# Performance work log

Hardware: AMD Instinct MI355X
Metric: run time of the kernel (lower is better)

The kernel has to match this reference:

```python
import math
import jax, jax.numpy as jnp
import numpy as np

B, T, S = 2, 2048, 2048
D_MODEL, N_HEADS = 1024, 16
HEAD_DIM = D_MODEL // N_HEADS
OUT_DIM = 1024


def setup_inputs() -> dict:
    key = jax.random.key(0)
    ks = jax.random.split(key, 6)
    q = jax.random.normal(ks[0], (B, T, D_MODEL), dtype=jnp.float32)
    k = jax.random.normal(ks[1], (B, S, D_MODEL), dtype=jnp.float32)
    v = jax.random.normal(ks[2], (B, S, D_MODEL), dtype=jnp.float32)
    rel_pos_bias = jax.random.normal(ks[3], (T, S, N_HEADS), dtype=jnp.float32)
    # shared qkv projection weight (torch ModuleList([Linear]*3) aliases one module)
    lim = 1.0 / math.sqrt(D_MODEL)
    Wqkv = jax.random.uniform(ks[4], (D_MODEL, D_MODEL), minval=-lim, maxval=lim, dtype=jnp.float32)
    Wout = jax.random.uniform(ks[5], (OUT_DIM, D_MODEL), minval=-lim, maxval=lim, dtype=jnp.float32)
    logit_scale = jnp.full((N_HEADS, 1, 1), math.log(10.0), dtype=jnp.float32)
    return {"q": q, "k": k, "v": v, "rel_pos_bias": rel_pos_bias,
            "Wqkv": Wqkv, "Wout": Wout, "logit_scale": logit_scale}


def _l2norm(x, eps=1e-12):
    # matches torch F.normalize(dim=-1)
    n = jnp.sqrt(jnp.sum(x * x, axis=-1, keepdims=True))
    return x / jnp.maximum(n, eps)


def reference(q, k, v, rel_pos_bias, Wqkv, Wout, logit_scale):
    # shared qkv projection (Linear, no bias): x @ W.T
    qp = q @ Wqkv.T
    kp = k @ Wqkv.T
    vp = v @ Wqkv.T
    # [B, H, T, Dh]
    qh = qp.reshape(B, T, N_HEADS, HEAD_DIM).transpose(0, 2, 1, 3)
    kh = kp.reshape(B, S, N_HEADS, HEAD_DIM).transpose(0, 2, 1, 3)
    vh = vp.reshape(B, S, N_HEADS, HEAD_DIM).transpose(0, 2, 1, 3)
    # cosine attention with clamped learned logit scale
    scale = jnp.exp(jnp.minimum(logit_scale, math.log(100.0)))  # [H,1,1]
    attn = jnp.einsum('bhtd,bhsd->bhts', _l2norm(qh), _l2norm(kh)) * scale
    # rel_pos_bias [T,S,H] -> [H,T,S], broadcast over batch
    attn = attn + rel_pos_bias.transpose(2, 0, 1)
    attn = jax.nn.softmax(attn, axis=-1)
    vals = jnp.einsum('bhts,bhsd->bhtd', attn, vh)
    vals = vals.transpose(0, 2, 1, 3).reshape(B, T, D_MODEL)
    return vals @ Wout.T
```

## Files before the change

### kernel.cpp

```cpp
#include <hip/hip_runtime.h>
#include <stdint.h>

typedef unsigned short u16;
using bf16x8 = __attribute__((ext_vector_type(8))) __bf16;
using f32x4  = __attribute__((ext_vector_type(4))) float;
using u16x8  = __attribute__((ext_vector_type(8))) u16;
using u16x4  = __attribute__((ext_vector_type(4))) u16;
using i32x4  = __attribute__((ext_vector_type(4))) int;

#define BB 2
#define TT 2048
#define SQ 2048
#define DM 1024
#define NH 16
#define HD 64
#define LOG2E 1.44269504088896340736f

__device__ __forceinline__ float bf2f(u16 u) {
  uint32_t x = ((uint32_t)u) << 16;
  return __builtin_bit_cast(float, x);
}
__device__ __forceinline__ u16 f2bf(float f) {
  uint32_t x = __builtin_bit_cast(uint32_t, f);
  x += 0x7fffu + ((x >> 16) & 1u);
  return (u16)(x >> 16);
}
__device__ __forceinline__ int cvt_pk_bf16(float lo, float hi) {
  int r;
  asm("v_cvt_pk_bf16_f32 %0, %1, %2" : "=v"(r) : "v"(lo), "v"(hi));
  return r;
}

typedef __attribute__((address_space(1))) void gvoid;
typedef __attribute__((address_space(3))) void lvoid;
__device__ __forceinline__ void g2l16(const void* g, void* l) {
  __builtin_amdgcn_global_load_lds((gvoid*)g, (lvoid*)l, 16, 0, 0);
}

__global__ __launch_bounds__(256) void convert_all(
    const float* __restrict__ q, const float* __restrict__ k,
    const float* __restrict__ v, const float* __restrict__ wq,
    const float* __restrict__ wo, u16* __restrict__ qc, u16* __restrict__ kc,
    u16* __restrict__ vc, u16* __restrict__ wqc, u16* __restrict__ woc) {
  const float* src;
  u16* dst;
  int n8;
  switch (blockIdx.y) {
    case 0:  src = q;  dst = qc;  n8 = 4096 * 1024 / 8; break;
    case 1:  src = k;  dst = kc;  n8 = 4096 * 1024 / 8; break;
    case 2:  src = v;  dst = vc;  n8 = 4096 * 1024 / 8; break;
    case 3:  src = wq; dst = wqc; n8 = 1024 * 1024 / 8; break;
    default: src = wo; dst = woc; n8 = 1024 * 1024 / 8; break;
  }
  int i = blockIdx.x * 256 + threadIdx.x;
  if (i >= n8) return;
  f32x4 a = ((const f32x4*)src)[(size_t)i * 2];
  f32x4 b = ((const f32x4*)src)[(size_t)i * 2 + 1];
  u16x8 o;
#pragma unroll
  for (int j = 0; j < 4; ++j) { o[j] = f2bf(a[j]); o[4 + j] = f2bf(b[j]); }
  ((u16x8*)dst)[i] = o;
}

template <typename OutT>
__device__ __forceinline__ void gemm_body(const u16* __restrict__ A,
                                          const u16* __restrict__ W,
                                          OutT* __restrict__ C,
                                          const float* __restrict__ ls,
                                          int norm_mode) {
  const int n0 = blockIdx.x * 128;
  const int m0 = blockIdx.y * 128;
  const int tid = threadIdx.x;
  const int w = tid >> 6, lane = tid & 63;
  const int l15 = lane & 15, lg = lane >> 4;
  const int wr = w >> 1, wc = w & 1;

  __shared__ u16 ldsA[16 * 512];
  __shared__ u16 ldsB[16 * 512];

  f32x4 acc[4][4];
#pragma unroll
  for (int i = 0; i < 4; ++i)
#pragma unroll
    for (int j = 0; j < 4; ++j) acc[i][j] = (f32x4){0.f, 0.f, 0.f, 0.f};

  for (int kt = 0; kt < 1024; kt += 64) {
#pragma unroll
    for (int u = 0; u < 4; ++u) {
      int f = w * 4 + u;
      int mt = f >> 1, ks = f & 1;
      g2l16(A + (size_t)(m0 + mt * 16 + l15) * 1024 + kt + ks * 32 + lg * 8,
            &ldsA[f * 512]);
      g2l16(W + (size_t)(n0 + mt * 16 + l15) * 1024 + kt + ks * 32 + lg * 8,
            &ldsB[f * 512]);
    }
    __syncthreads();
#pragma unroll
    for (int ks = 0; ks < 2; ++ks) {
      bf16x8 a[4], b[4];
#pragma unroll
      for (int i = 0; i < 4; ++i)
        a[i] = *(const bf16x8*)&ldsA[((wr * 4 + i) * 2 + ks) * 512 + lane * 8];
#pragma unroll
      for (int j = 0; j < 4; ++j)
        b[j] = *(const bf16x8*)&ldsB[((wc * 4 + j) * 2 + ks) * 512 + lane * 8];
#pragma unroll
      for (int i = 0; i < 4; ++i)
#pragma unroll
        for (int j = 0; j < 4; ++j)
          acc[i][j] = __builtin_amdgcn_mfma_f32_16x16x32_bf16(a[i], b[j],
                                                              acc[i][j], 0, 0, 0);
    }
    __syncthreads();
  }

  if (norm_mode < 2) {
    float sc = 1.0f;
    if (norm_mode == 0)
      sc = __expf(fminf(ls[(n0 >> 6) + wc], 4.60517019f)) * LOG2E;
#pragma unroll
    for (int i = 0; i < 4; ++i)
#pragma unroll
      for (int r = 0; r < 4; ++r) {
        float ss = 0.f;
#pragma unroll
        for (int j = 0; j < 4; ++j) ss += acc[i][j][r] * acc[i][j][r];
#pragma unroll
        for (int d = 1; d < 16; d <<= 1) ss += __shfl_xor(ss, d, 64);
        float f = sc / fmaxf(sqrtf(ss), 1e-12f);
#pragma unroll
        for (int j = 0; j < 4; ++j) acc[i][j][r] *= f;
      }
  }

#pragma unroll
  for (int i = 0; i < 4; ++i) {
    int row0 = m0 + (wr * 4 + i) * 16 + lg * 4;
#pragma unroll
    for (int j = 0; j < 4; ++j) {
      int col = n0 + (wc * 4 + j) * 16 + l15;
#pragma unroll
      for (int r = 0; r < 4; ++r) {
        if constexpr (sizeof(OutT) == 2)
          C[(size_t)(row0 + r) * 1024 + col] = f2bf(acc[i][j][r]);
        else
          C[(size_t)(row0 + r) * 1024 + col] = acc[i][j][r];
      }
    }
  }
}

__global__ __launch_bounds__(256, 2) void gemm_qkv(
    const u16* __restrict__ q, const u16* __restrict__ k,
    const u16* __restrict__ v, const u16* __restrict__ W,
    const float* __restrict__ ls,
    u16* __restrict__ qp, u16* __restrict__ kp, u16* __restrict__ vp) {
  const u16* A;
  u16* C;
  if (blockIdx.z == 0) { A = q; C = qp; }
  else if (blockIdx.z == 1) { A = k; C = kp; }
  else { A = v; C = vp; }
  gemm_body<u16>(A, W, C, ls, blockIdx.z);
}

__global__ __launch_bounds__(256, 2) void gemm_out(const u16* __restrict__ A,
                                                   const u16* __restrict__ W,
                                                   float* __restrict__ C) {
  gemm_body<float>(A, W, C, nullptr, 2);
}

__global__ __launch_bounds__(256) void transpose_v(const u16* __restrict__ vp,
                                                   u16* __restrict__ vt) {
  int st = blockIdx.x;
  int bh = blockIdx.y;
  __shared__ u16 lds[64][72];
  int tid = threadIdx.x;
  int s = tid >> 2, c0 = (tid & 3) * 16;
  int b = bh >> 4, h = bh & 15;
  const u16* src = vp + (size_t)(b * SQ + st * 64 + s) * 1024 + h * 64 + c0;
  u16x8 r0 = *(const u16x8*)src;
  u16x8 r1 = *(const u16x8*)(src + 8);
#pragma unroll
  for (int j = 0; j < 8; ++j) { lds[s][c0 + j] = r0[j]; lds[s][c0 + 8 + j] = r1[j]; }
  __syncthreads();
  int d = tid >> 2, sc = (tid & 3) * 16;
  u16x8 o0, o1;
#pragma unroll
  for (int j = 0; j < 8; ++j) { o0[j] = lds[sc + j][d]; o1[j] = lds[sc + 8 + j][d]; }
  u16* dst = vt + (size_t)(bh * 64 + d) * SQ + st * 64 + sc;
  *(u16x8*)dst = o0;
  *((u16x8*)(dst + 8)) = o1;
}

__global__ __launch_bounds__(256) void transpose_bias(const float* __restrict__ bias,
                                                      u16* __restrict__ bt) {
  int t = blockIdx.y;
  int s0 = blockIdx.x * 512;
  __shared__ u16 lds[16][520];
  int tid = threadIdx.x;
  const float* src = bias + ((size_t)t * SQ + s0 + tid * 2) * 16;
  float v[32];
#pragma unroll
  for (int j = 0; j < 8; ++j) {
    f32x4 r = ((const f32x4*)src)[j];
#pragma unroll
    for (int e = 0; e < 4; ++e) v[j * 4 + e] = r[e];
  }
  int sl = tid * 2;
#pragma unroll
  for (int e = 0; e < 32; ++e) lds[e & 15][sl + (e >> 4)] = f2bf(v[e] * LOG2E);
  __syncthreads();
  int h = tid >> 4, sc = (tid & 15) * 32;
  u16* dst = bt + ((size_t)h * TT + t) * SQ + s0 + sc;
#pragma unroll
  for (int j = 0; j < 4; ++j) {
    u16x8 o;
#pragma unroll
    for (int e = 0; e < 8; ++e) o[e] = lds[h][sc + j * 8 + e];
    *((u16x8*)(dst + j * 8)) = o;
  }
}

__global__ __launch_bounds__(256, 2) void flash_attn(
    const u16* __restrict__ qn, const u16* __restrict__ kn,
    const u16* __restrict__ vt, const u16* __restrict__ bt,
    u16* __restrict__ av) {
  const int h = blockIdx.x >> 1, b = blockIdx.x & 1, qt = blockIdx.y;
  const int tid = threadIdx.x, w = tid >> 6, lane = tid & 63;
  const int l15 = lane & 15, lg = lane >> 4;

  __shared__ u16 ldsK[2][16 * 512];
  __shared__ u16 ldsV[2][16 * 512];

  const int t0 = qt * 64 + w * 16;

  bf16x8 qf[2];
  {
    const u16* qb = qn + (size_t)(b * TT + t0 + l15) * 1024 + h * 64 + lg * 8;
    qf[0] = *(const bf16x8*)qb;
    qf[1] = *(const bf16x8*)(qb + 32);
  }

  f32x4 o[4];
#pragma unroll
  for (int n = 0; n < 4; ++n) o[n] = (f32x4){0.f, 0.f, 0.f, 0.f};
  float li = 0.f;

  const u16* kb = kn + (size_t)(b * SQ) * 1024 + h * 64;
  const u16* vb = vt + (size_t)((b * NH + h) * 64) * SQ;
  const u16* bbl = bt + ((size_t)h * TT + t0 + l15) * SQ + lg * 4;

#define STAGE(bufi, stg)                                                       \
  {                                                                            \
    _Pragma("unroll") for (int u_ = 0; u_ < 4; ++u_) {                         \
      int f_ = w * 4 + u_;                                                     \
      int nt_ = f_ >> 1, ks_ = f_ & 1;                                         \
      g2l16(kb + (size_t)((stg) + nt_ * 16 + l15) * 1024 + ks_ * 32 + lg * 8,  \
            &ldsK[bufi][f_ * 512]);                                            \
      int j_ = f_ >> 2, k2_ = f_ & 3;                                          \
      g2l16(vb + (size_t)(j_ * 16 + l15) * SQ + (stg) + k2_ * 32 + lg * 8,     \
            &ldsV[bufi][f_ * 512]);                                            \
    }                                                                          \
  }

  STAGE(0, 0);

  for (int it = 0; it < 16; ++it) {
    const int cur = it & 1;
    const int st = it * 128;

    u16x4 bv[8];
#pragma unroll
    for (int nt = 0; nt < 8; ++nt)
      bv[nt] = *(const u16x4*)(bbl + st + nt * 16);
    asm volatile("" ::: "memory");

    if (it < 15) {
      STAGE(cur ^ 1, st + 128);
      asm volatile("s_waitcnt vmcnt(16)" ::: "memory");
    } else {
      asm volatile("s_waitcnt vmcnt(8)" ::: "memory");
    }
    __builtin_amdgcn_s_barrier();

    f32x4 sacc[8];
#pragma unroll
    for (int nt = 0; nt < 8; ++nt) {
      sacc[nt] = (f32x4){0.f, 0.f, 0.f, 0.f};
#pragma unroll
      for (int ks = 0; ks < 2; ++ks)
        sacc[nt] = __builtin_amdgcn_mfma_f32_16x16x32_bf16(
            *(const bf16x8*)&ldsK[cur][(nt * 2 + ks) * 512 + lane * 8],
            qf[ks], sacc[nt], 0, 0, 0);
    }

    int pk[8][2];
#pragma unroll
    for (int nt = 0; nt < 8; ++nt) {
      float p0 = __builtin_amdgcn_exp2f(sacc[nt][0] + bf2f(bv[nt][0]));
      float p1 = __builtin_amdgcn_exp2f(sacc[nt][1] + bf2f(bv[nt][1]));
      float p2 = __builtin_amdgcn_exp2f(sacc[nt][2] + bf2f(bv[nt][2]));
      float p3 = __builtin_amdgcn_exp2f(sacc[nt][3] + bf2f(bv[nt][3]));
      li += (p0 + p1) + (p2 + p3);
      pk[nt][0] = cvt_pk_bf16(p0, p1);
      pk[nt][1] = cvt_pk_bf16(p2, p3);
    }

#pragma unroll
    for (int ks2 = 0; ks2 < 4; ++ks2) {
      auto a0 = __builtin_amdgcn_permlane32_swap(pk[2 * ks2][0],
                                                 pk[2 * ks2 + 1][0], false, false);
      auto w0 = __builtin_amdgcn_permlane16_swap(a0[0], a0[1], false, false);
      auto a1 = __builtin_amdgcn_permlane32_swap(pk[2 * ks2][1],
                                                 pk[2 * ks2 + 1][1], false, false);
      auto w1 = __builtin_amdgcn_permlane16_swap(a1[0], a1[1], false, false);
      i32x4 pw = (i32x4){(int)w0[0], (int)w1[0], (int)w0[1], (int)w1[1]};
      bf16x8 pf = __builtin_bit_cast(bf16x8, pw);
#pragma unroll
      for (int j = 0; j < 4; ++j)
        o[j] = __builtin_amdgcn_mfma_f32_16x16x32_bf16(
            pf, *(const bf16x8*)&ldsV[cur][(j * 4 + ks2) * 512 + lane * 8],
            o[j], 0, 0, 0);
    }
    if (it < 15) __builtin_amdgcn_s_barrier();
  }
#undef STAGE

  li += __shfl_xor(li, 16, 64);
  li += __shfl_xor(li, 32, 64);
  float inv[4];
#pragma unroll
  for (int r = 0; r < 4; ++r) inv[r] = 1.0f / __shfl(li, lg * 4 + r, 64);

#pragma unroll
  for (int j = 0; j < 4; ++j)
#pragma unroll
    for (int r = 0; r < 4; ++r) {
      size_t row = (size_t)(b * TT + t0 + lg * 4 + r);
      av[row * 1024 + h * 64 + j * 16 + l15] = f2bf(o[j][r] * inv[r]);
    }
}

extern "C" void kernel_launch(void* const* d_in, const int* in_sizes, int n_in,
                              void* d_out, int out_size, void* d_ws, size_t ws_size,
                              hipStream_t stream) {
  const float* q    = (const float*)d_in[0];
  const float* k    = (const float*)d_in[1];
  const float* v    = (const float*)d_in[2];
  const float* bias = (const float*)d_in[3];
  const float* Wqkv = (const float*)d_in[4];
  const float* Wout = (const float*)d_in[5];
  const float* ls   = (const float*)d_in[6];
  float* out = (float*)d_out;

  char* ws = (char*)d_ws;
  u16* qc = (u16*)(ws);
  u16* kc = (u16*)(ws + (size_t)(8  << 20));
  u16* vc = (u16*)(ws + (size_t)(16 << 20));
  u16* Wq = (u16*)(ws + (size_t)(24 << 20));
  u16* Wo = (u16*)(ws + (size_t)(26 << 20));
  u16* qn = (u16*)(ws + (size_t)(28 << 20));
  u16* kn = (u16*)(ws + (size_t)(36 << 20));
  u16* av = (u16*)(ws + (size_t)(44 << 20));
  u16* vtb = (u16*)(ws + (size_t)(52 << 20));
  u16* bt  = (u16*)(ws + (size_t)(60 << 20));

  dim3 blk(256);
  transpose_bias<<<dim3(4, 2048), blk, 0, stream>>>(bias, bt);
  convert_all<<<dim3(2048, 5), blk, 0, stream>>>(q, k, v, Wqkv, Wout,
                                                 qc, kc, vc, Wq, Wo);

  gemm_qkv<<<dim3(8, 32, 3), blk, 0, stream>>>(qc, kc, vc, Wq, ls, qn, kn, av);
  transpose_v<<<dim3(32, 32), blk, 0, stream>>>(av, vtb);
  flash_attn<<<dim3(32, 32), blk, 0, stream>>>(qn, kn, vtb, bt, av);
  gemm_out<<<dim3(8, 32), blk, 0, stream>>>(av, Wo, out);
}
```

Before: 650.1 us.

## Merge both batches into one 512-thread attention block; coalesce bias transpose loads

The flash attention kernel now processes both batch elements for one head and query tile in a single 512-thread block, with separate K/V LDS buffers per batch. The likely aim is to share each bias tile read between the two batches within one block and to halve the block count. The bias transpose kernel also changes its read pattern so adjacent threads load consecutive 16-byte chunks, giving coalesced global reads. LDS use per block doubles, which may limit occupancy, and the barriers now synchronise eight waves instead of four.

After: 672.7 us. +3.5%, slower.

```diff
diff --git a/kernel.cpp b/kernel.cpp
--- a/kernel.cpp
+++ b/kernel.cpp
@@ -198,17 +198,16 @@
   int s0 = blockIdx.x * 512;
   __shared__ u16 lds[16][520];
   int tid = threadIdx.x;
-  const float* src = bias + ((size_t)t * SQ + s0 + tid * 2) * 16;
-  float v[32];
-#pragma unroll
-  for (int j = 0; j < 8; ++j) {
-    f32x4 r = ((const f32x4*)src)[j];
-#pragma unroll
-    for (int e = 0; e < 4; ++e) v[j * 4 + e] = r[e];
-  }
-  int sl = tid * 2;
-#pragma unroll
-  for (int e = 0; e < 32; ++e) lds[e & 15][sl + (e >> 4)] = f2bf(v[e] * LOG2E);
+  const float* src = bias + ((size_t)t * SQ + s0) * 16;
+  int h0 = (tid & 3) * 4;
+  int sr = tid >> 2;
+#pragma unroll
+  for (int p = 0; p < 8; ++p) {
+    f32x4 r = *(const f32x4*)(src + p * 1024 + tid * 4);
+#pragma unroll
+    for (int e = 0; e < 4; ++e)
+      lds[h0 + e][p * 64 + sr] = f2bf(r[e] * LOG2E);
+  }
   __syncthreads();
   int h = tid >> 4, sc = (tid & 15) * 32;
   u16* dst = bt + ((size_t)h * TT + t) * SQ + s0 + sc;
@@ -221,16 +220,18 @@
   }
 }
 
-__global__ __launch_bounds__(256, 2) void flash_attn(
+__global__ __launch_bounds__(512, 2) void flash_attn(
     const u16* __restrict__ qn, const u16* __restrict__ kn,
     const u16* __restrict__ vt, const u16* __restrict__ bt,
     u16* __restrict__ av) {
-  const int h = blockIdx.x >> 1, b = blockIdx.x & 1, qt = blockIdx.y;
-  const int tid = threadIdx.x, w = tid >> 6, lane = tid & 63;
+  const int h = blockIdx.x, qt = blockIdx.y;
+  const int tid = threadIdx.x, lane = tid & 63;
+  const int wAll = tid >> 6;
+  const int b = wAll >> 2, w = wAll & 3;
   const int l15 = lane & 15, lg = lane >> 4;
 
-  __shared__ u16 ldsK[2][16 * 512];
-  __shared__ u16 ldsV[2][16 * 512];
+  __shared__ u16 ldsK[2][2][16 * 512];
+  __shared__ u16 ldsV[2][2][16 * 512];
 
   const int t0 = qt * 64 + w * 16;
 
@@ -256,10 +257,10 @@
       int f_ = w * 4 + u_;                                                     \
       int nt_ = f_ >> 1, ks_ = f_ & 1;                                         \
       g2l16(kb + (size_t)((stg) + nt_ * 16 + l15) * 1024 + ks_ * 32 + lg * 8,  \
-            &ldsK[bufi][f_ * 512]);                                            \
+            &ldsK[bufi][b][f_ * 512]);                                         \
       int j_ = f_ >> 2, k2_ = f_ & 3;                                          \
       g2l16(vb + (size_t)(j_ * 16 + l15) * SQ + (stg) + k2_ * 32 + lg * 8,     \
-            &ldsV[bufi][f_ * 512]);                                            \
+            &ldsV[bufi][b][f_ * 512]);                                         \
     }                                                                          \
   }
 
@@ -290,7 +291,7 @@
 #pragma unroll
       for (int ks = 0; ks < 2; ++ks)
         sacc[nt] = __builtin_amdgcn_mfma_f32_16x16x32_bf16(
-            *(const bf16x8*)&ldsK[cur][(nt * 2 + ks) * 512 + lane * 8],
+            *(const bf16x8*)&ldsK[cur][b][(nt * 2 + ks) * 512 + lane * 8],
             qf[ks], sacc[nt], 0, 0, 0);
     }
 
@@ -319,7 +320,7 @@
 #pragma unroll
       for (int j = 0; j < 4; ++j)
         o[j] = __builtin_amdgcn_mfma_f32_16x16x32_bf16(
-            pf, *(const bf16x8*)&ldsV[cur][(j * 4 + ks2) * 512 + lane * 8],
+            pf, *(const bf16x8*)&ldsV[cur][b][(j * 4 + ks2) * 512 + lane * 8],
             o[j], 0, 0, 0);
     }
     if (it < 15) __builtin_amdgcn_s_barrier();
@@ -372,6 +373,6 @@
 
   gemm_qkv<<<dim3(8, 32, 3), blk, 0, stream>>>(qc, kc, vc, Wq, ls, qn, kn, av);
   transpose_v<<<dim3(32, 32), blk, 0, stream>>>(av, vtb);
-  flash_attn<<<dim3(32, 32), blk, 0, stream>>>(qn, kn, vtb, bt, av);
+  flash_attn<<<dim3(16, 32), dim3(512), 0, stream>>>(qn, kn, vtb, bt, av);
   gemm_out<<<dim3(8, 32), blk, 0, stream>>>(av, Wo, out);
 }
```
